# Kernel optimization log

Measured on AMD Instinct MI355X. Metric: run time of the kernel, lower is better.

## Reference

```python
import jax, jax.numpy as jnp
import numpy as np

NUM_LEVELS = 8
BASE_H = 512
BASE_W = 512
CHANNELS = 16
N_QUERIES = 1000000


def _resize_bilinear(tex, h, w):
    """PyTorch F.interpolate(mode='bilinear', align_corners=False). tex: (C,H,W) -> (C,h,w)."""
    C, H, W = tex.shape

    def coords(out_size, in_size):
        # half-pixel source coords, clamped at 0 like PyTorch
        src = (jnp.arange(out_size, dtype=jnp.float32) + 0.5) * (in_size / out_size) - 0.5
        src = jnp.maximum(src, 0.0)
        i0 = jnp.minimum(jnp.floor(src).astype(jnp.int32), in_size - 1)
        i1 = jnp.minimum(i0 + 1, in_size - 1)
        t = src - i0.astype(jnp.float32)
        return i0, i1, t

    y0, y1, ty = coords(h, H)
    x0, x1, tx = coords(w, W)
    rows = tex[:, y0, :] * (1.0 - ty)[None, :, None] + tex[:, y1, :] * ty[None, :, None]  # (C,h,W)
    out = rows[:, :, x0] * (1.0 - tx) + rows[:, :, x1] * tx  # (C,h,w)
    return out


def _grid_sample(tex, gx, gy):
    """PyTorch F.grid_sample(mode='bilinear', padding_mode='border', align_corners=True).
    tex: (C,h,w); gx,gy: (N,) in [-1,1]. Returns (N,C)."""
    C, h, w = tex.shape
    x = jnp.clip((gx + 1.0) * 0.5 * (w - 1), 0.0, w - 1)
    y = jnp.clip((gy + 1.0) * 0.5 * (h - 1), 0.0, h - 1)
    x0 = jnp.clip(jnp.floor(x).astype(jnp.int32), 0, w - 1)
    y0 = jnp.clip(jnp.floor(y).astype(jnp.int32), 0, h - 1)
    x1 = jnp.minimum(x0 + 1, w - 1)
    y1 = jnp.minimum(y0 + 1, h - 1)
    fx = x - x0.astype(x.dtype)
    fy = y - y0.astype(y.dtype)
    v00 = tex[:, y0, x0]  # (C,N)
    v01 = tex[:, y0, x1]
    v10 = tex[:, y1, x0]
    v11 = tex[:, y1, x1]
    out = (v00 * (1 - fx) * (1 - fy) + v01 * fx * (1 - fy)
           + v10 * (1 - fx) * fy + v11 * fx * fy)  # (C,N)
    return out.T  # (N,C)


def setup_inputs() -> dict:
    key = jax.random.key(0)
    k1, k2, k3 = jax.random.split(key, 3)
    uv = jax.random.uniform(k1, (N_QUERIES, 2), dtype=jnp.float32)
    p = jax.random.uniform(k2, (N_QUERIES,), dtype=jnp.float32)
    tex = jax.random.normal(k3, (1, CHANNELS, BASE_H, BASE_W), dtype=jnp.float32) * 0.01
    return {"uv": uv, "p": p, "tex": tex}


def reference(uv, p, tex):
    tex2 = tex[0]  # (C,H,W)
    gx = 2.0 * uv[:, 0] - 1.0
    gy = 2.0 * uv[:, 1] - 1.0
    levels = []
    for i in range(NUM_LEVELS):
        h = max(BASE_H >> i, 1)
        w = max(BASE_W >> i, 1)
        t = _resize_bilinear(tex2, h, w)
        levels.append(_grid_sample(t, gx, gy))  # (N,C)
    big = jnp.stack(levels, axis=1)  # (N,L,C)
    lf = p * (NUM_LEVELS - 1)
    l0 = jnp.floor(lf).astype(jnp.int32)
    l1 = jnp.minimum(l0 + 1, NUM_LEVELS - 1)
    alpha = (lf - l0.astype(lf.dtype))[:, None]  # (N,1)
    out0 = jnp.take_along_axis(big, l0[:, None, None], axis=1)[:, 0]  # (N,C)
    out1 = jnp.take_along_axis(big, l1[:, None, None], axis=1)[:, 0]
    return out0 * (1.0 - alpha) + out1 * alpha
```

## Files before the change

kernel.cpp:

```cpp
#include <hip/hip_runtime.h>
#include <hip/hip_fp16.h>

static constexpr int BASE = 512;

typedef float f32x2 __attribute__((ext_vector_type(2)));
typedef float f32x4 __attribute__((ext_vector_type(4)));
typedef unsigned int u32x4 __attribute__((ext_vector_type(4)));

__constant__ int c_off[8] = {0, 4194304, 5242880, 5505024, 5570560, 5586944, 5591040, 5592064};

__global__ void transpose_l0(const float* __restrict__ tex, __half* __restrict__ dst) {
    int pix = blockIdx.x * blockDim.x + threadIdx.x;
    float v[16];
#pragma unroll
    for (int c = 0; c < 16; ++c)
        v[c] = __builtin_nontemporal_load(tex + c * 262144 + pix);
    __half2 h[8];
#pragma unroll
    for (int i = 0; i < 8; ++i) h[i] = __floats2half2_rn(v[2 * i], v[2 * i + 1]);
    float4* o = (float4*)(dst + (size_t)pix * 16);
    o[0] = *(const float4*)&h[0];
    o[1] = *(const float4*)&h[4];
}

__device__ inline void load_texel16(const __half* p, float* f) {
    float4 r0 = ((const float4*)p)[0];
    float4 r1 = ((const float4*)p)[1];
    const __half2* h0 = (const __half2*)&r0;
    const __half2* h1 = (const __half2*)&r1;
#pragma unroll
    for (int i = 0; i < 4; ++i) {
        float2 a = __half22float2(h0[i]);
        f[2 * i] = a.x; f[2 * i + 1] = a.y;
        float2 b = __half22float2(h1[i]);
        f[8 + 2 * i] = b.x; f[9 + 2 * i] = b.y;
    }
}

__global__ void build_levels(const __half* __restrict__ l0, __half* __restrict__ ws) {
    int lev = blockIdx.y + 1;
    int w = BASE >> lev;
    int npix = w * w;
    int pix = blockIdx.x * blockDim.x + threadIdx.x;
    if (pix >= npix) return;
    int y = pix >> (9 - lev);
    int x = pix & (w - 1);
    int xx = (x << lev) + (1 << (lev - 1)) - 1;
    int yy = (y << lev) + (1 << (lev - 1)) - 1;
    const __half* b00 = l0 + (size_t)(yy * 512 + xx) * 16;
    float a[16], b[16], c[16], d[16];
    load_texel16(b00, a);
    load_texel16(b00 + 16, b);
    load_texel16(b00 + 512 * 16, c);
    load_texel16(b00 + 512 * 16 + 16, d);
    __half2 r[8];
#pragma unroll
    for (int i = 0; i < 8; ++i) {
        float r0 = (a[2 * i] * 0.5f + c[2 * i] * 0.5f) * 0.5f +
                   (b[2 * i] * 0.5f + d[2 * i] * 0.5f) * 0.5f;
        float r1 = (a[2 * i + 1] * 0.5f + c[2 * i + 1] * 0.5f) * 0.5f +
                   (b[2 * i + 1] * 0.5f + d[2 * i + 1] * 0.5f) * 0.5f;
        r[i] = __floats2half2_rn(r0, r1);
    }
    float4* dst = (float4*)(ws + c_off[lev] + (size_t)pix * 16);
    dst[0] = *(const float4*)&r[0];
    dst[1] = *(const float4*)&r[4];
}

__global__ __launch_bounds__(256, 8)
void sample_kernel(const float2* __restrict__ uv, const float* __restrict__ p,
                   const __half* __restrict__ ws, float* __restrict__ out, int N) {
    int tid = blockIdx.x * blockDim.x + threadIdx.x;
    int n = tid >> 1;
    int q = tid & 1;
    if (n >= N) return;

    f32x2 uvn = __builtin_nontemporal_load((const f32x2*)uv + n);
    float pp = __builtin_nontemporal_load(p + n);
    float gx = 2.0f * uvn.x - 1.0f;
    float gy = 2.0f * uvn.y - 1.0f;

    float lf = pp * 7.0f;
    int l0 = min((int)lf, 7);
    int l1 = min(l0 + 1, 7);
    float alpha = lf - (float)l0;

    int off[8];
    float wgt[8];
    int ls2[2] = {l0, l1};
    float lw2[2] = {1.0f - alpha, alpha};
#pragma unroll
    for (int k = 0; k < 2; ++k) {
        int l = ls2[k];
        int w = BASE >> l;
        float wm1 = (float)(w - 1);
        float x = fminf(fmaxf((gx + 1.0f) * 0.5f * wm1, 0.0f), wm1);
        float y = fminf(fmaxf((gy + 1.0f) * 0.5f * wm1, 0.0f), wm1);
        int x0 = min((int)x, w - 1);
        int y0 = min((int)y, w - 1);
        int x1 = min(x0 + 1, w - 1);
        int y1 = min(y0 + 1, w - 1);
        float fx = x - (float)x0;
        float fy = y - (float)y0;
        int sh = 24 - 2 * l;
        int offh = (0x555555 >> sh) << sh;
        int base = (offh << 1) + q * 16;
        off[4 * k + 0] = base + (y0 * w + x0) * 32;
        off[4 * k + 1] = base + (y0 * w + x1) * 32;
        off[4 * k + 2] = base + (y1 * w + x0) * 32;
        off[4 * k + 3] = base + (y1 * w + x1) * 32;
        wgt[4 * k + 0] = (1.0f - fx) * (1.0f - fy) * lw2[k];
        wgt[4 * k + 1] = fx * (1.0f - fy) * lw2[k];
        wgt[4 * k + 2] = (1.0f - fx) * fy * lw2[k];
        wgt[4 * k + 3] = fx * fy * lw2[k];
    }

    u32x4 srsrc;
    unsigned long long wsa = (unsigned long long)(const void*)ws;
    srsrc.x = (unsigned int)wsa;
    srsrc.y = (unsigned int)(wsa >> 32);
    srsrc.z = 0xFFFFFFFFu;
    srsrc.w = 0x00020000u;

    float4 r0, r1, r2, r3, r4, r5, r6, r7;
    asm volatile(
        "buffer_load_dwordx4 %0, %8, %16, 0 offen\n\t"
        "buffer_load_dwordx4 %1, %9, %16, 0 offen\n\t"
        "buffer_load_dwordx4 %2, %10, %16, 0 offen\n\t"
        "buffer_load_dwordx4 %3, %11, %16, 0 offen\n\t"
        "buffer_load_dwordx4 %4, %12, %16, 0 offen\n\t"
        "buffer_load_dwordx4 %5, %13, %16, 0 offen\n\t"
        "buffer_load_dwordx4 %6, %14, %16, 0 offen\n\t"
        "buffer_load_dwordx4 %7, %15, %16, 0 offen\n\t"
        "s_waitcnt vmcnt(4)"
        : "=&v"(r0), "=&v"(r1), "=&v"(r2), "=&v"(r3),
          "=&v"(r4), "=&v"(r5), "=&v"(r6), "=&v"(r7)
        : "v"(off[0]), "v"(off[1]), "v"(off[2]), "v"(off[3]),
          "v"(off[4]), "v"(off[5]), "v"(off[6]), "v"(off[7]),
          "s"(srsrc));

    float acc[8];
#pragma unroll
    for (int j = 0; j < 8; ++j) acc[j] = 0.0f;

#define ACCUM(R, I)                                            \
    {                                                          \
        const __half2* h = (const __half2*)&(R);               \
        float wv = wgt[I];                                     \
        _Pragma("unroll")                                      \
        for (int j = 0; j < 4; ++j) {                          \
            float2 a = __half22float2(h[j]);                   \
            acc[2 * j]     += a.x * wv;                        \
            acc[2 * j + 1] += a.y * wv;                        \
        }                                                      \
    }
    ACCUM(r0, 0) ACCUM(r1, 1) ACCUM(r2, 2) ACCUM(r3, 3)

    asm volatile("s_waitcnt vmcnt(0)" ::: "memory");
    __builtin_amdgcn_sched_barrier(0);

    ACCUM(r4, 4) ACCUM(r5, 5) ACCUM(r6, 6) ACCUM(r7, 7)
#undef ACCUM

    f32x4 o0 = {acc[0], acc[1], acc[2], acc[3]};
    f32x4 o1 = {acc[4], acc[5], acc[6], acc[7]};
    f32x4* o = (f32x4*)(out + (size_t)n * 16 + 8 * q);
    __builtin_nontemporal_store(o0, o);
    __builtin_nontemporal_store(o1, o + 1);
}

extern "C" void kernel_launch(void* const* d_in, const int* in_sizes, int n_in,
                              void* d_out, int out_size, void* d_ws, size_t ws_size,
                              hipStream_t stream) {
    const float* uv  = (const float*)d_in[0];
    const float* p   = (const float*)d_in[1];
    const float* tex = (const float*)d_in[2];
    float* out = (float*)d_out;
    __half* ws = (__half*)d_ws;
    int N = in_sizes[1];

    transpose_l0<<<262144 / 256, 256, 0, stream>>>(tex, ws);

    dim3 gA2(256, 7);
    build_levels<<<gA2, 256, 0, stream>>>(ws, ws);

    long long total = (long long)N * 2;
    int blocks = (int)((total + 255) / 256);
    sample_kernel<<<blocks, 256, 0, stream>>>((const float2*)uv, p, ws, out, N);
}
```

Measured before the change: 126.7 us.

## Stage coarse mip levels in LDS and make sampling kernel persistent

Copies mip levels 4-7 (about 43 KB of fp16 texels) into shared memory at block start and serves bilinear taps for those levels from LDS, selecting between LDS and buffer-load results per level. The sampling kernel becomes a grid-stride persistent loop over 768 blocks of 512 threads. This aims to cut global/L2 traffic for the small hot levels, but adds a per-block LDS fill, LDS-limited occupancy, and still issues dummy buffer loads for LDS-served taps.

```diff
diff --git a/kernel.cpp b/kernel.cpp
--- a/kernel.cpp
+++ b/kernel.cpp
@@ -8,6 +8,9 @@
 typedef unsigned int u32x4 __attribute__((ext_vector_type(4)));
 
 __constant__ int c_off[8] = {0, 4194304, 5242880, 5505024, 5570560, 5586944, 5591040, 5592064};
+static constexpr int LVL4_HALF = 5570560;
+static constexpr int LVL4_BYTE = 11141120;
+static constexpr int SMEM_F4 = 2720;
 
 __global__ void transpose_l0(const float* __restrict__ tex, __half* __restrict__ dst) {
     int pix = blockIdx.x * blockDim.x + threadIdx.x;
@@ -67,53 +70,16 @@
     dst[1] = *(const float4*)&r[4];
 }
 
-__global__ __launch_bounds__(256, 8)
+__global__ __launch_bounds__(512, 6)
 void sample_kernel(const float2* __restrict__ uv, const float* __restrict__ p,
-                   const __half* __restrict__ ws, float* __restrict__ out, int N) {
-    int tid = blockIdx.x * blockDim.x + threadIdx.x;
-    int n = tid >> 1;
-    int q = tid & 1;
-    if (n >= N) return;
-
-    f32x2 uvn = __builtin_nontemporal_load((const f32x2*)uv + n);
-    float pp = __builtin_nontemporal_load(p + n);
-    float gx = 2.0f * uvn.x - 1.0f;
-    float gy = 2.0f * uvn.y - 1.0f;
-
-    float lf = pp * 7.0f;
-    int l0 = min((int)lf, 7);
-    int l1 = min(l0 + 1, 7);
-    float alpha = lf - (float)l0;
-
-    int off[8];
-    float wgt[8];
-    int ls2[2] = {l0, l1};
-    float lw2[2] = {1.0f - alpha, alpha};
-#pragma unroll
-    for (int k = 0; k < 2; ++k) {
-        int l = ls2[k];
-        int w = BASE >> l;
-        float wm1 = (float)(w - 1);
-        float x = fminf(fmaxf((gx + 1.0f) * 0.5f * wm1, 0.0f), wm1);
-        float y = fminf(fmaxf((gy + 1.0f) * 0.5f * wm1, 0.0f), wm1);
-        int x0 = min((int)x, w - 1);
-        int y0 = min((int)y, w - 1);
-        int x1 = min(x0 + 1, w - 1);
-        int y1 = min(y0 + 1, w - 1);
-        float fx = x - (float)x0;
-        float fy = y - (float)y0;
-        int sh = 24 - 2 * l;
-        int offh = (0x555555 >> sh) << sh;
-        int base = (offh << 1) + q * 16;
-        off[4 * k + 0] = base + (y0 * w + x0) * 32;
-        off[4 * k + 1] = base + (y0 * w + x1) * 32;
-        off[4 * k + 2] = base + (y1 * w + x0) * 32;
-        off[4 * k + 3] = base + (y1 * w + x1) * 32;
-        wgt[4 * k + 0] = (1.0f - fx) * (1.0f - fy) * lw2[k];
-        wgt[4 * k + 1] = fx * (1.0f - fy) * lw2[k];
-        wgt[4 * k + 2] = (1.0f - fx) * fy * lw2[k];
-        wgt[4 * k + 3] = fx * fy * lw2[k];
-    }
+                   const __half* __restrict__ ws, float* __restrict__ out, int total) {
+    __shared__ __align__(16) float4 smem[SMEM_F4];
+
+    {
+        const float4* src = (const float4*)(ws + LVL4_HALF);
+        for (int i = threadIdx.x; i < SMEM_F4; i += 512) smem[i] = src[i];
+    }
+    __syncthreads();
 
     u32x4 srsrc;
     unsigned long long wsa = (unsigned long long)(const void*)ws;
@@ -122,30 +88,91 @@
     srsrc.z = 0xFFFFFFFFu;
     srsrc.w = 0x00020000u;
 
-    float4 r0, r1, r2, r3, r4, r5, r6, r7;
-    asm volatile(
-        "buffer_load_dwordx4 %0, %8, %16, 0 offen\n\t"
-        "buffer_load_dwordx4 %1, %9, %16, 0 offen\n\t"
-        "buffer_load_dwordx4 %2, %10, %16, 0 offen\n\t"
-        "buffer_load_dwordx4 %3, %11, %16, 0 offen\n\t"
-        "buffer_load_dwordx4 %4, %12, %16, 0 offen\n\t"
-        "buffer_load_dwordx4 %5, %13, %16, 0 offen\n\t"
-        "buffer_load_dwordx4 %6, %14, %16, 0 offen\n\t"
-        "buffer_load_dwordx4 %7, %15, %16, 0 offen\n\t"
-        "s_waitcnt vmcnt(4)"
-        : "=&v"(r0), "=&v"(r1), "=&v"(r2), "=&v"(r3),
-          "=&v"(r4), "=&v"(r5), "=&v"(r6), "=&v"(r7)
-        : "v"(off[0]), "v"(off[1]), "v"(off[2]), "v"(off[3]),
-          "v"(off[4]), "v"(off[5]), "v"(off[6]), "v"(off[7]),
-          "s"(srsrc));
-
-    float acc[8];
-#pragma unroll
-    for (int j = 0; j < 8; ++j) acc[j] = 0.0f;
-
-#define ACCUM(R, I)                                            \
+    const char* sb = (const char*)smem;
+    int stride = gridDim.x * blockDim.x;
+
+    for (int tid = blockIdx.x * blockDim.x + threadIdx.x; tid < total; tid += stride) {
+        int n = tid >> 1;
+        int q = tid & 1;
+
+        f32x2 uvn = __builtin_nontemporal_load((const f32x2*)uv + n);
+        float pp = __builtin_nontemporal_load(p + n);
+        float gx = 2.0f * uvn.x - 1.0f;
+        float gy = 2.0f * uvn.y - 1.0f;
+
+        float lf = pp * 7.0f;
+        int l0 = min((int)lf, 7);
+        int l1 = min(l0 + 1, 7);
+        float alpha = lf - (float)l0;
+
+        int goff[8];
+        int loff[8];
+        float wgt[8];
+        bool sel[2];
+        int ls2[2] = {l0, l1};
+        float lw2[2] = {1.0f - alpha, alpha};
+#pragma unroll
+        for (int k = 0; k < 2; ++k) {
+            int l = ls2[k];
+            int w = BASE >> l;
+            float wm1 = (float)(w - 1);
+            float x = fminf(fmaxf((gx + 1.0f) * 0.5f * wm1, 0.0f), wm1);
+            float y = fminf(fmaxf((gy + 1.0f) * 0.5f * wm1, 0.0f), wm1);
+            int x0 = min((int)x, w - 1);
+            int y0 = min((int)y, w - 1);
+            int x1 = min(x0 + 1, w - 1);
+            int y1 = min(y0 + 1, w - 1);
+            float fx = x - (float)x0;
+            float fy = y - (float)y0;
+            int sh = 24 - 2 * l;
+            int offh = (0x555555 >> sh) << sh;
+            bool s = l >= 4;
+            sel[k] = s;
+            int base = offh * 2 + q * 16;
+            int ob0 = base + (y0 * w + x0) * 32;
+            int ob1 = base + (y0 * w + x1) * 32;
+            int ob2 = base + (y1 * w + x0) * 32;
+            int ob3 = base + (y1 * w + x1) * 32;
+            goff[4 * k + 0] = s ? 0 : ob0;
+            goff[4 * k + 1] = s ? 0 : ob1;
+            goff[4 * k + 2] = s ? 0 : ob2;
+            goff[4 * k + 3] = s ? 0 : ob3;
+            loff[4 * k + 0] = s ? (ob0 - LVL4_BYTE) : 0;
+            loff[4 * k + 1] = s ? (ob1 - LVL4_BYTE) : 0;
+            loff[4 * k + 2] = s ? (ob2 - LVL4_BYTE) : 0;
+            loff[4 * k + 3] = s ? (ob3 - LVL4_BYTE) : 0;
+            wgt[4 * k + 0] = (1.0f - fx) * (1.0f - fy) * lw2[k];
+            wgt[4 * k + 1] = fx * (1.0f - fy) * lw2[k];
+            wgt[4 * k + 2] = (1.0f - fx) * fy * lw2[k];
+            wgt[4 * k + 3] = fx * fy * lw2[k];
+        }
+
+        float4 r0, r1, r2, r3, r4, r5, r6, r7;
+        asm volatile(
+            "buffer_load_dwordx4 %0, %8, %16, 0 offen\n\t"
+            "buffer_load_dwordx4 %1, %9, %16, 0 offen\n\t"
+            "buffer_load_dwordx4 %2, %10, %16, 0 offen\n\t"
+            "buffer_load_dwordx4 %3, %11, %16, 0 offen\n\t"
+            "buffer_load_dwordx4 %4, %12, %16, 0 offen\n\t"
+            "buffer_load_dwordx4 %5, %13, %16, 0 offen\n\t"
+            "buffer_load_dwordx4 %6, %14, %16, 0 offen\n\t"
+            "buffer_load_dwordx4 %7, %15, %16, 0 offen\n\t"
+            "s_waitcnt vmcnt(4)"
+            : "=&v"(r0), "=&v"(r1), "=&v"(r2), "=&v"(r3),
+              "=&v"(r4), "=&v"(r5), "=&v"(r6), "=&v"(r7)
+            : "v"(goff[0]), "v"(goff[1]), "v"(goff[2]), "v"(goff[3]),
+              "v"(goff[4]), "v"(goff[5]), "v"(goff[6]), "v"(goff[7]),
+              "s"(srsrc));
+
+        float acc[8];
+#pragma unroll
+        for (int j = 0; j < 8; ++j) acc[j] = 0.0f;
+
+#define ACCUM_SEL(RG, LOFF, I, S)                              \
     {                                                          \
-        const __half2* h = (const __half2*)&(R);               \
+        float4 vl_ = *(const float4*)(sb + (LOFF));            \
+        float4 v_ = (S) ? vl_ : (RG);                          \
+        const __half2* h = (const __half2*)&v_;                \
         float wv = wgt[I];                                     \
         _Pragma("unroll")                                      \
         for (int j = 0; j < 4; ++j) {                          \
@@ -154,19 +181,26 @@
             acc[2 * j + 1] += a.y * wv;                        \
         }                                                      \
     }
-    ACCUM(r0, 0) ACCUM(r1, 1) ACCUM(r2, 2) ACCUM(r3, 3)
-
-    asm volatile("s_waitcnt vmcnt(0)" ::: "memory");
-    __builtin_amdgcn_sched_barrier(0);
-
-    ACCUM(r4, 4) ACCUM(r5, 5) ACCUM(r6, 6) ACCUM(r7, 7)
-#undef ACCUM
-
-    f32x4 o0 = {acc[0], acc[1], acc[2], acc[3]};
-    f32x4 o1 = {acc[4], acc[5], acc[6], acc[7]};
-    f32x4* o = (f32x4*)(out + (size_t)n * 16 + 8 * q);
-    __builtin_nontemporal_store(o0, o);
-    __builtin_nontemporal_store(o1, o + 1);
+        ACCUM_SEL(r0, loff[0], 0, sel[0])
+        ACCUM_SEL(r1, loff[1], 1, sel[0])
+        ACCUM_SEL(r2, loff[2], 2, sel[0])
+        ACCUM_SEL(r3, loff[3], 3, sel[0])
+
+        asm volatile("s_waitcnt vmcnt(0)" ::: "memory");
+        __builtin_amdgcn_sched_barrier(0);
+
+        ACCUM_SEL(r4, loff[4], 4, sel[1])
+        ACCUM_SEL(r5, loff[5], 5, sel[1])
+        ACCUM_SEL(r6, loff[6], 6, sel[1])
+        ACCUM_SEL(r7, loff[7], 7, sel[1])
+#undef ACCUM_SEL
+
+        f32x4 o0 = {acc[0], acc[1], acc[2], acc[3]};
+        f32x4 o1 = {acc[4], acc[5], acc[6], acc[7]};
+        f32x4* o = (f32x4*)(out + (size_t)n * 16 + 8 * q);
+        __builtin_nontemporal_store(o0, o);
+        __builtin_nontemporal_store(o1, o + 1);
+    }
 }
 
 extern "C" void kernel_launch(void* const* d_in, const int* in_sizes, int n_in,
@@ -185,6 +219,6 @@
     build_levels<<<gA2, 256, 0, stream>>>(ws, ws);
 
     long long total = (long long)N * 2;
-    int blocks = (int)((total + 255) / 256);
-    sample_kernel<<<blocks, 256, 0, stream>>>((const float2*)uv, p, ws, out, N);
-}
+    int blocks = (int)min((long long)768, (total + 511) / 512);
+    sample_kernel<<<blocks, 512, 0, stream>>>((const float2*)uv, p, ws, out, (int)total);
+}
```

Measured after the change: 131.7 us. 1.04x slower.
